# Kernel tuning notes

Hardware: AMD Instinct MI355X
Metric: run time of the kernel (lower is better)

Reference implementation:

```python
import jax, jax.numpy as jnp
import numpy as np

N_NODES = 50000
N_EDGES = 1600000


def setup_inputs() -> dict:
    key = jax.random.key(0)
    ks = jax.random.split(key, 12)
    x = jax.random.normal(ks[0], (N_NODES, 128), dtype=jnp.float32)
    edge_index = jax.random.randint(ks[1], (2, N_EDGES), 0, N_NODES, dtype=jnp.int32)
    edge_weight = jax.random.uniform(ks[2], (N_EDGES,), dtype=jnp.float32)
    K = 3
    def glorot(k, kk, cin, cout):
        s = (6.0 / (cin + cout)) ** 0.5
        return jax.random.uniform(k, (kk, cin, cout), dtype=jnp.float32, minval=-s, maxval=s)
    W0 = glorot(ks[3], K, 128, 128); b0 = jnp.zeros((128,), jnp.float32)
    W1 = glorot(ks[4], K, 128, 128); b1 = jnp.zeros((128,), jnp.float32)
    W2 = glorot(ks[5], K, 128, 64);  b2 = jnp.zeros((64,), jnp.float32)
    return {"x": x, "edge_index": edge_index, "edge_weight": edge_weight,
            "W0": W0, "b0": b0, "W1": W1, "b1": b1, "W2": W2, "b2": b2}


def _laplacian_norm(edge_index, edge_weight, n_nodes):
    # PyG ChebConv with lambda_max=2.0, sym normalization:
    # L_hat = 2*(I - D^-1/2 A D^-1/2)/lambda_max - I = -D^-1/2 A D^-1/2 (zero diag)
    src, dst = edge_index[0], edge_index[1]
    deg = jax.ops.segment_sum(edge_weight, src, num_segments=n_nodes)
    dinv = jnp.where(deg > 0, jax.lax.rsqrt(jnp.maximum(deg, 1e-30)), 0.0)
    return -dinv[src] * edge_weight * dinv[dst]


def _spmm(norm, src, dst, x, n_nodes):
    # out[i] = sum_{e: dst[e]=i} norm[e] * x[src[e]]
    return jax.ops.segment_sum(norm[:, None] * x[src], dst, num_segments=n_nodes)


def _cheb_conv(x, src, dst, norm, W, b, n_nodes):
    K = W.shape[0]
    out = jnp.einsum('nc,cd->nd', x, W[0])
    tx0 = x
    tx1 = _spmm(norm, src, dst, x, n_nodes)  # L_hat @ x
    out = out + jnp.einsum('nc,cd->nd', tx1, W[1])
    for k in range(2, K):
        tx2 = 2.0 * _spmm(norm, src, dst, tx1, n_nodes) - tx0
        out = out + jnp.einsum('nc,cd->nd', tx2, W[k])
        tx0, tx1 = tx1, tx2
    return out + b


def reference(x, edge_index, edge_weight, W0, b0, W1, b1, W2, b2):
    n_nodes = x.shape[0]
    src, dst = edge_index[0], edge_index[1]
    norm = _laplacian_norm(edge_index, edge_weight, n_nodes)
    h = jax.nn.sigmoid(_cheb_conv(x, src, dst, norm, W0, b0, n_nodes))
    h = jax.nn.sigmoid(_cheb_conv(h, src, dst, norm, W1, b1, n_nodes))
    return jax.nn.sigmoid(_cheb_conv(h, src, dst, norm, W2, b2, n_nodes))
```

## Files before the change

kernel.cpp:

```cpp
#include <hip/hip_runtime.h>
#include <hip/hip_fp16.h>
#include <math.h>

#define N_NODES 50000
#define N_EDGES 1600000
#define NBUCK 196
#define EBLK 400
#define CHUNK 4000

typedef _Float16 f16x8 __attribute__((ext_vector_type(8)));
typedef _Float16 f16x4 __attribute__((ext_vector_type(4)));
typedef _Float16 f16x2 __attribute__((ext_vector_type(2)));
typedef float f32x4 __attribute__((ext_vector_type(4)));

union HBits { __half h; unsigned short u; };

__global__ __launch_bounds__(256) void k_bcount(const int* __restrict__ src,
                                                const int* __restrict__ dst,
                                                int* __restrict__ bcnt_d,
                                                int* __restrict__ bcnt_s) {
    __shared__ int lcd[256];
    __shared__ int lcs[256];
    int tid = threadIdx.x;
    lcd[tid] = 0; lcs[tid] = 0;
    __syncthreads();
    int base = blockIdx.x * CHUNK;
    for (int i = tid; i < CHUNK; i += 256) {
        atomicAdd(&lcd[dst[base + i] >> 8], 1);
        atomicAdd(&lcs[src[base + i] >> 8], 1);
    }
    __syncthreads();
    bcnt_d[blockIdx.x * 256 + tid] = lcd[tid];
    bcnt_s[blockIdx.x * 256 + tid] = lcs[tid];
}

__global__ __launch_bounds__(256) void k_bscan1(int* __restrict__ bcnt_d,
                                                int* __restrict__ bcnt_s,
                                                int* __restrict__ btot) {
    int b = blockIdx.x & 255;
    int* bcnt = (blockIdx.x >> 8) ? bcnt_s : bcnt_d;
    int tid = threadIdx.x;
    int k0 = 2 * tid;
    int v0 = (k0 < EBLK) ? bcnt[k0 * 256 + b] : 0;
    int v1 = (k0 + 1 < EBLK) ? bcnt[(k0 + 1) * 256 + b] : 0;
    int pair = v0 + v1;
    __shared__ int s[256];
    s[tid] = pair;
    __syncthreads();
    for (int off = 1; off < 256; off <<= 1) {
        int t = (tid >= off) ? s[tid - off] : 0;
        __syncthreads();
        s[tid] += t;
        __syncthreads();
    }
    int excl = s[tid] - pair;
    if (k0 < EBLK)     bcnt[k0 * 256 + b] = excl;
    if (k0 + 1 < EBLK) bcnt[(k0 + 1) * 256 + b] = excl + v0;
    if (tid == 255) btot[(blockIdx.x >> 8) * 256 + b] = s[255];
}

__global__ __launch_bounds__(256) void k_bscan2(const int* __restrict__ btot,
                                                int* __restrict__ bstart_d,
                                                int* __restrict__ bstart_s,
                                                int* __restrict__ row_start) {
    __shared__ int s[256];
    int b = threadIdx.x;
    int v = btot[b];
    s[b] = v;
    __syncthreads();
    for (int off = 1; off < 256; off <<= 1) {
        int t = (b >= off) ? s[b - off] : 0;
        __syncthreads();
        s[b] += t;
        __syncthreads();
    }
    bstart_d[b] = s[b] - v;
    if (b == 0) {
        bstart_d[256] = N_EDGES;
        row_start[N_NODES] = N_EDGES;
    }
    __syncthreads();
    int v2 = btot[256 + b];
    s[b] = v2;
    __syncthreads();
    for (int off = 1; off < 256; off <<= 1) {
        int t = (b >= off) ? s[b - off] : 0;
        __syncthreads();
        s[b] += t;
        __syncthreads();
    }
    bstart_s[b] = s[b] - v2;
    if (b == 0) bstart_s[256] = N_EDGES;
}

__global__ __launch_bounds__(256) void k_bscatter(const int* __restrict__ src,
                                                  const int* __restrict__ dst,
                                                  const float* __restrict__ w,
                                                  const int* __restrict__ bcnt_d,
                                                  const int* __restrict__ bcnt_s,
                                                  const int* __restrict__ bstart_d,
                                                  const int* __restrict__ bstart_s,
                                                  uint2* __restrict__ dsw,
                                                  unsigned* __restrict__ ssw) {
    __shared__ int curd[256];
    __shared__ int curs[256];
    int tid = threadIdx.x;
    curd[tid] = bcnt_d[blockIdx.x * 256 + tid] + bstart_d[tid];
    curs[tid] = bcnt_s[blockIdx.x * 256 + tid] + bstart_s[tid];
    __syncthreads();
    int base = blockIdx.x * CHUNK;
    for (int i = tid; i < CHUNK; i += 256) {
        int d = dst[base + i];
        int ss = src[base + i];
        float wi = w[base + i];
        int p = atomicAdd(&curd[d >> 8], 1);
        uint2 r; r.x = (unsigned)ss | ((unsigned)(d & 255) << 16);
        r.y = __float_as_uint(wi);
        dsw[p] = r;
        int q = atomicAdd(&curs[ss >> 8], 1);
        HBits hw; hw.h = __float2half(wi);
        ssw[q] = (unsigned)(ss & 255) | ((unsigned)hw.u << 16);
    }
}

__global__ __launch_bounds__(256) void k_sdeg(const unsigned* __restrict__ ssw,
                                              const int* __restrict__ bstart_s,
                                              float* __restrict__ dinv) {
    __shared__ float h[256];
    int tid = threadIdx.x;
    int b = blockIdx.x;
    h[tid] = 0.f;
    __syncthreads();
    int e0 = bstart_s[b], e1 = bstart_s[b + 1];
    for (int i = e0 + tid; i < e1; i += 256) {
        unsigned r = ssw[i];
        HBits hb; hb.u = (unsigned short)(r >> 16);
        atomicAdd(&h[r & 255], __half2float(hb.h));
    }
    __syncthreads();
    int node = (b << 8) + tid;
    if (node < N_NODES) {
        float d = h[tid];
        dinv[node] = d > 0.f ? rsqrtf(fmaxf(d, 1e-30f)) : 0.f;
    }
}

__global__ __launch_bounds__(256) void k_bcsr(const uint2* __restrict__ dsw,
                                              const int* __restrict__ bstart_d,
                                              const float* __restrict__ dinv,
                                              int* __restrict__ row_start,
                                              unsigned* __restrict__ csr4) {
    __shared__ int ncnt[256];
    __shared__ int cur[256];
    __shared__ int sc[256];
    __shared__ float ldinv[256];
    int tid = threadIdx.x;
    int b = blockIdx.x;
    int node = (b << 8) + tid;
    ncnt[tid] = 0;
    ldinv[tid] = (node < N_NODES) ? dinv[node] : 0.f;
    __syncthreads();
    int e0 = bstart_d[b], e1 = bstart_d[b + 1];
    for (int i = e0 + tid; i < e1; i += 256)
        atomicAdd(&ncnt[(dsw[i].x >> 16) & 255], 1);
    __syncthreads();
    int v = ncnt[tid];
    sc[tid] = v;
    __syncthreads();
    for (int off = 1; off < 256; off <<= 1) {
        int t = (tid >= off) ? sc[tid - off] : 0;
        __syncthreads();
        sc[tid] += t;
        __syncthreads();
    }
    int excl = sc[tid] - v;
    cur[tid] = excl;
    if (node < N_NODES) row_start[node] = e0 + excl;
    __syncthreads();
    for (int i = e0 + tid; i < e1; i += 256) {
        uint2 sw = dsw[i];
        int srcn = sw.x & 0xFFFF;
        int ld = (sw.x >> 16) & 255;
        int p = e0 + atomicAdd(&cur[ld], 1);
        float nv = -dinv[srcn] * __uint_as_float(sw.y) * ldinv[ld];
        HBits hb; hb.h = __float2half(nv);
        csr4[p] = (unsigned)srcn | ((unsigned)hb.u << 16);
    }
}

__global__ void k_cvt_x(const float* __restrict__ x, __half* __restrict__ X, int n4) {
    int i = blockIdx.x * blockDim.x + threadIdx.x;
    if (i < n4) {
        float4 v = *(const float4*)&x[(size_t)i * 4];
        f16x4 o;
        o[0] = (_Float16)v.x; o[1] = (_Float16)v.y;
        o[2] = (_Float16)v.z; o[3] = (_Float16)v.w;
        *(f16x4*)&X[(size_t)i * 4] = o;
    }
}

__global__ void k_wt(const float* __restrict__ W, __half* __restrict__ Wt, int C) {
    int i = blockIdx.x * blockDim.x + threadIdx.x;
    if (i < 3 * C * 128) {
        int n = i >> 7, k = i & 127;
        int slice = n / C, c = n % C;
        float v;
        if (slice == 0)      v = 2.f * W[(size_t)(256 + k) * C + c];
        else if (slice == 1) v = W[(size_t)(128 + k) * C + c];
        else                 v = W[(size_t)k * C + c] - W[(size_t)(256 + k) * C + c];
        Wt[i] = __float2half(v);
    }
}

template <int ST_IN, int ST_ADD, int ST_OUT, int FW, int SIG, int F32>
__global__ __launch_bounds__(256) void k_spmm(const __half* __restrict__ Xin,
                                              const __half* __restrict__ Add,
                                              void* __restrict__ outp,
                                              const float* __restrict__ bias,
                                              const int* __restrict__ row_start,
                                              const unsigned* __restrict__ csr4) {
    constexpr int NL = FW / 8;
    constexpr int EG = 64 / NL;
    constexpr int KP2 = 16 / EG;
    int node = blockIdx.x * 4 + (threadIdx.x >> 6);
    int lane = threadIdx.x & 63;
    int eg = lane / NL;
    int fs = lane % NL;
    int s = row_start[node];
    int e = row_start[node + 1];
    const unsigned* cb = csr4 + eg;
    const __half* Tbase = Xin + fs * 8;
    float acc[8];
    #pragma unroll
    for (int f = 0; f < 8; f++) acc[f] = 0.f;

    int j = s;
    for (; j + 32 <= e; j += 32) {
        unsigned ea[KP2], eb[KP2];
        #pragma unroll
        for (int k = 0; k < KP2; k++) {
            ea[k] = cb[j + 2 * EG * k];
            eb[k] = cb[j + 2 * EG * k + EG];
        }
        f16x8 r0[KP2], r1[KP2]; f16x2 nv2[KP2];
        #pragma unroll
        for (int k = 0; k < KP2; k++) {
            int sp0 = (int)(ea[k] & 0xFFFFu);
            int sp1 = (int)(eb[k] & 0xFFFFu);
            r0[k] = *(const f16x8*)&Tbase[(size_t)sp0 * ST_IN];
            r1[k] = *(const f16x8*)&Tbase[(size_t)sp1 * ST_IN];
            unsigned np = (ea[k] >> 16) | (eb[k] & 0xFFFF0000u);
            __builtin_memcpy(&nv2[k], &np, 4);
        }
        #pragma unroll
        for (int k = 0; k < KP2; k++)
            #pragma unroll
            for (int f = 0; f < 8; f++) {
                f16x2 h; h[0] = r0[k][f]; h[1] = r1[k][f];
                acc[f] = __builtin_amdgcn_fdot2(h, nv2[k], acc[f], false);
            }
    }
    if (j + 16 <= e) {
        unsigned ea[KP2 / 2], eb[KP2 / 2];
        #pragma unroll
        for (int k = 0; k < KP2 / 2; k++) {
            ea[k] = cb[j + 2 * EG * k];
            eb[k] = cb[j + 2 * EG * k + EG];
        }
        #pragma unroll
        for (int k = 0; k < KP2 / 2; k++) {
            int sp0 = (int)(ea[k] & 0xFFFFu);
            int sp1 = (int)(eb[k] & 0xFFFFu);
            f16x8 r0 = *(const f16x8*)&Tbase[(size_t)sp0 * ST_IN];
            f16x8 r1 = *(const f16x8*)&Tbase[(size_t)sp1 * ST_IN];
            unsigned np = (ea[k] >> 16) | (eb[k] & 0xFFFF0000u);
            f16x2 nv; __builtin_memcpy(&nv, &np, 4);
            #pragma unroll
            for (int f = 0; f < 8; f++) {
                f16x2 h; h[0] = r0[f]; h[1] = r1[f];
                acc[f] = __builtin_amdgcn_fdot2(h, nv, acc[f], false);
            }
        }
        j += 16;
    }
    if (j < e) {
        #pragma unroll
        for (int k = 0; k < KP2 / 2; k++) {
            int i0 = j + 2 * EG * k + eg;
            int i1 = i0 + EG;
            unsigned va = csr4[min(i0, e - 1)];
            unsigned vb = csr4[min(i1, e - 1)];
            int sp0 = (int)(va & 0xFFFFu);
            int sp1 = (int)(vb & 0xFFFFu);
            unsigned np = (va >> 16) | (vb & 0xFFFF0000u);
            if (i0 >= e) np &= 0xFFFF0000u;
            if (i1 >= e) np &= 0x0000FFFFu;
            f16x2 nv; __builtin_memcpy(&nv, &np, 4);
            f16x8 r0 = *(const f16x8*)&Tbase[(size_t)sp0 * ST_IN];
            f16x8 r1 = *(const f16x8*)&Tbase[(size_t)sp1 * ST_IN];
            #pragma unroll
            for (int f = 0; f < 8; f++) {
                f16x2 h; h[0] = r0[f]; h[1] = r1[f];
                acc[f] = __builtin_amdgcn_fdot2(h, nv, acc[f], false);
            }
        }
    }
    #pragma unroll
    for (int f = 0; f < 8; f++)
        for (int m = NL; m < 64; m <<= 1)
            acc[f] += __shfl_xor(acc[f], m);
    if (eg == 0) {
        f16x8 av = *(const f16x8*)&Add[(size_t)node * ST_ADD + fs * 8];
        float v[8];
        #pragma unroll
        for (int f = 0; f < 8; f++) v[f] = acc[f] + (float)av[f];
        if (SIG) {
            #pragma unroll
            for (int f = 0; f < 8; f++) {
                v[f] += bias[fs * 8 + f];
                v[f] = 1.f / (1.f + expf(-v[f]));
            }
        }
        if (F32) {
            float* o = (float*)outp + (size_t)node * ST_OUT + fs * 8;
            float4 o0; o0.x = v[0]; o0.y = v[1]; o0.z = v[2]; o0.w = v[3];
            float4 o1; o1.x = v[4]; o1.y = v[5]; o1.z = v[6]; o1.w = v[7];
            *(float4*)&o[0] = o0;
            *(float4*)&o[4] = o1;
        } else {
            f16x8 o;
            #pragma unroll
            for (int f = 0; f < 8; f++) o[f] = (_Float16)v[f];
            *(f16x8*)((__half*)outp + (size_t)node * ST_OUT + fs * 8) = o;
        }
    }
}

template <int CC, int STG>
__global__ __launch_bounds__(256) void k_gemm(const __half* __restrict__ A,
                                              const __half* __restrict__ Wt,
                                              __half* __restrict__ G, int M) {
    constexpr int N3 = 3 * CC;
    constexpr int NF = N3 / 16;
    __shared__ _Float16 As[64][40];
    __shared__ _Float16 Bs[N3][40];
    int tid = threadIdx.x;
    int wave = tid >> 6, lane = tid & 63;
    int lm = lane & 15, lq = lane >> 4;
    int m0 = blockIdx.x * 64;
    f32x4 acc[NF];
    for (int nf = 0; nf < NF; nf++) acc[nf] = (f32x4)0.0f;

    for (int k0 = 0; k0 < 128; k0 += 32) {
        {
            int r = tid >> 2, q = tid & 3;
            int row = m0 + r;
            if (row >= M) row = M - 1;
            *(f16x8*)&As[r][q * 8] = *(const f16x8*)&A[(size_t)row * 128 + k0 + q * 8];
        }
        for (int i = 0; i < N3 / 64; i++) {
            int idx = tid + i * 256;
            int n = idx >> 2, q = idx & 3;
            *(f16x8*)&Bs[n][q * 8] = *(const f16x8*)&Wt[(size_t)n * 128 + k0 + q * 8];
        }
        __syncthreads();
        f16x8 a = *(const f16x8*)&As[wave * 16 + lm][lq * 8];
        for (int nf = 0; nf < NF; nf++) {
            f16x8 b = *(const f16x8*)&Bs[nf * 16 + lm][lq * 8];
            acc[nf] = __builtin_amdgcn_mfma_f32_16x16x32_f16(a, b, acc[nf], 0, 0, 0);
        }
        __syncthreads();
    }
    for (int nf = 0; nf < NF; nf++) {
        for (int r = 0; r < 4; r++) {
            int grow = m0 + wave * 16 + lq * 4 + r;
            int col = nf * 16 + lm;
            if (grow < M)
                G[(size_t)grow * STG + col] = __float2half(acc[nf][r]);
        }
    }
}

extern "C" void kernel_launch(void* const* d_in, const int* in_sizes, int n_in,
                              void* d_out, int out_size, void* d_ws, size_t ws_size,
                              hipStream_t stream) {
    const float* x  = (const float*)d_in[0];
    const int*   ei = (const int*)d_in[1];
    const float* ew = (const float*)d_in[2];
    const float* W0 = (const float*)d_in[3];
    const float* b0 = (const float*)d_in[4];
    const float* W1 = (const float*)d_in[5];
    const float* b1 = (const float*)d_in[6];
    const float* W2 = (const float*)d_in[7];
    const float* b2 = (const float*)d_in[8];
    const int* src = ei;
    const int* dst = ei + N_EDGES;

    char* ws = (char*)d_ws;
    size_t off = 0;
    auto alloc = [&](size_t bytes) -> char* {
        size_t p = (off + 255) & ~(size_t)255;
        off = p + bytes;
        return ws + p;
    };
    __half*   X      = (__half*)alloc((size_t)N_NODES * 128 * 2);
    __half*   G      = (__half*)alloc((size_t)N_NODES * 512 * 2);
    __half*   TMP    = (__half*)alloc((size_t)N_NODES * 128 * 2);
    unsigned* csr4   = (unsigned*)alloc((size_t)N_EDGES * 4);
    uint2*    dsw    = (uint2*)alloc((size_t)N_EDGES * 8);
    unsigned* ssw    = (unsigned*)alloc((size_t)N_EDGES * 4);
    int*      bcnt_d = (int*)alloc((size_t)EBLK * 256 * 4);
    int*      bcnt_s = (int*)alloc((size_t)EBLK * 256 * 4);
    int*      btot   = (int*)alloc(512 * 4);
    int*      bstart_d = (int*)alloc(257 * 4);
    int*      bstart_s = (int*)alloc(257 * 4);
    int*      row_start= (int*)alloc((size_t)(N_NODES + 1) * 4);
    float*    dinv   = (float*)alloc((size_t)N_NODES * 4);
    __half*   Wt0    = (__half*)alloc((size_t)384 * 128 * 2);
    __half*   Wt1    = (__half*)alloc((size_t)384 * 128 * 2);
    __half*   Wt2    = (__half*)alloc((size_t)192 * 128 * 2);

    k_bcount<<<EBLK, 256, 0, stream>>>(src, dst, bcnt_d, bcnt_s);
    k_bscan1<<<512, 256, 0, stream>>>(bcnt_d, bcnt_s, btot);
    k_bscan2<<<1, 256, 0, stream>>>(btot, bstart_d, bstart_s, row_start);
    k_bscatter<<<EBLK, 256, 0, stream>>>(src, dst, ew, bcnt_d, bcnt_s,
                                         bstart_d, bstart_s, dsw, ssw);
    k_sdeg<<<NBUCK, 256, 0, stream>>>(ssw, bstart_s, dinv);
    k_bcsr<<<NBUCK, 256, 0, stream>>>(dsw, bstart_d, dinv, row_start, csr4);

    k_cvt_x<<<(N_NODES * 32 + 255) / 256, 256, 0, stream>>>(x, X, N_NODES * 32);
    k_wt<<<(3 * 128 * 128 + 255) / 256, 256, 0, stream>>>(W0, Wt0, 128);
    k_wt<<<(3 * 128 * 128 + 255) / 256, 256, 0, stream>>>(W1, Wt1, 128);
    k_wt<<<(3 * 64 * 128 + 255) / 256, 256, 0, stream>>>(W2, Wt2, 64);

    int gb = (N_NODES + 63) / 64;
    int sb = N_NODES / 4;
    k_gemm<128, 512><<<gb, 256, 0, stream>>>(X, Wt0, G, N_NODES);
    k_spmm<512, 512, 128, 128, 0, 0><<<sb, 256, 0, stream>>>(G, G + 128, TMP,
                                                             nullptr, row_start, csr4);
    k_spmm<128, 512, 128, 128, 1, 0><<<sb, 256, 0, stream>>>(TMP, G + 256, X,
                                                             b0, row_start, csr4);
    k_gemm<128, 512><<<gb, 256, 0, stream>>>(X, Wt1, G, N_NODES);
    k_spmm<512, 512, 128, 128, 0, 0><<<sb, 256, 0, stream>>>(G, G + 128, TMP,
                                                             nullptr, row_start, csr4);
    k_spmm<128, 512, 128, 128, 1, 0><<<sb, 256, 0, stream>>>(TMP, G + 256, X,
                                                             b1, row_start, csr4);
    k_gemm<64, 256><<<gb, 256, 0, stream>>>(X, Wt2, G, N_NODES);
    k_spmm<256, 256, 64, 64, 0, 0><<<sb, 256, 0, stream>>>(G, G + 64, TMP,
                                                           nullptr, row_start, csr4);
    k_spmm<64, 256, 64, 64, 1, 1><<<sb, 256, 0, stream>>>(TMP, G + 128, d_out,
                                                          b2, row_start, csr4);
}
```

Before: 494.6 us.

## Pad CSR rows to multiples of eight and vectorize edge loads in SpMM

Each node's CSR row is padded to a multiple of 8 entries, with zero-weight filler entries and per-bucket slack. Row offsets and padded lengths are stored as a uint2 per node, which lets the SpMM read edges with aligned uint4/uint2 vector loads and drop the masked, clamped tail path. The three weight-transform kernels and the x conversion are also merged into one prep launch. The cost is a slightly larger CSR array and extra gathers of node 0 for the padding entries.

```diff
diff --git a/kernel.cpp b/kernel.cpp
--- a/kernel.cpp
+++ b/kernel.cpp
@@ -7,6 +7,7 @@
 #define NBUCK 196
 #define EBLK 400
 #define CHUNK 4000
+#define CSR_CAP (N_EDGES + 2048 * NBUCK + 4096)
 
 typedef _Float16 f16x8 __attribute__((ext_vector_type(8)));
 typedef _Float16 f16x4 __attribute__((ext_vector_type(4)));
@@ -61,8 +62,7 @@
 
 __global__ __launch_bounds__(256) void k_bscan2(const int* __restrict__ btot,
                                                 int* __restrict__ bstart_d,
-                                                int* __restrict__ bstart_s,
-                                                int* __restrict__ row_start) {
+                                                int* __restrict__ bstart_s) {
     __shared__ int s[256];
     int b = threadIdx.x;
     int v = btot[b];
@@ -75,10 +75,7 @@
         __syncthreads();
     }
     bstart_d[b] = s[b] - v;
-    if (b == 0) {
-        bstart_d[256] = N_EDGES;
-        row_start[N_NODES] = N_EDGES;
-    }
+    if (b == 0) bstart_d[256] = N_EDGES;
     __syncthreads();
     int v2 = btot[256 + b];
     s[b] = v2;
@@ -148,7 +145,7 @@
 __global__ __launch_bounds__(256) void k_bcsr(const uint2* __restrict__ dsw,
                                               const int* __restrict__ bstart_d,
                                               const float* __restrict__ dinv,
-                                              int* __restrict__ row_start,
+                                              uint2* __restrict__ ri,
                                               unsigned* __restrict__ csr4) {
     __shared__ int ncnt[256];
     __shared__ int cur[256];
@@ -165,7 +162,8 @@
         atomicAdd(&ncnt[(dsw[i].x >> 16) & 255], 1);
     __syncthreads();
     int v = ncnt[tid];
-    sc[tid] = v;
+    int pc = (v + 7) & ~7;
+    sc[tid] = pc;
     __syncthreads();
     for (int off = 1; off < 256; off <<= 1) {
         int t = (tid >= off) ? sc[tid - off] : 0;
@@ -173,42 +171,74 @@
         sc[tid] += t;
         __syncthreads();
     }
-    int excl = sc[tid] - v;
+    int excl = sc[tid] - pc;
     cur[tid] = excl;
-    if (node < N_NODES) row_start[node] = e0 + excl;
+    int pbase = ((e0 + 7) & ~7) + 2048 * b;
+    if (node < N_NODES) {
+        uint2 r; r.x = (unsigned)(pbase + excl); r.y = (unsigned)pc;
+        ri[node] = r;
+    }
     __syncthreads();
     for (int i = e0 + tid; i < e1; i += 256) {
         uint2 sw = dsw[i];
         int srcn = sw.x & 0xFFFF;
         int ld = (sw.x >> 16) & 255;
-        int p = e0 + atomicAdd(&cur[ld], 1);
+        int p = pbase + atomicAdd(&cur[ld], 1);
         float nv = -dinv[srcn] * __uint_as_float(sw.y) * ldinv[ld];
         HBits hb; hb.h = __float2half(nv);
         csr4[p] = (unsigned)srcn | ((unsigned)hb.u << 16);
     }
-}
-
-__global__ void k_cvt_x(const float* __restrict__ x, __half* __restrict__ X, int n4) {
-    int i = blockIdx.x * blockDim.x + threadIdx.x;
-    if (i < n4) {
+    __syncthreads();
+    int st = pbase + excl;
+    for (int i = v; i < pc; i++) csr4[st + i] = 0u;
+}
+
+__device__ inline void wt_one(const float* __restrict__ W, __half* __restrict__ Wt,
+                              int C, int i) {
+    int n = i >> 7, k = i & 127;
+    int slice = n / C, c = n % C;
+    float v;
+    if (slice == 0)      v = 2.f * W[(size_t)(256 + k) * C + c];
+    else if (slice == 1) v = W[(size_t)(128 + k) * C + c];
+    else                 v = W[(size_t)k * C + c] - W[(size_t)(256 + k) * C + c];
+    Wt[i] = __float2half(v);
+}
+
+__global__ __launch_bounds__(256) void k_prep(const float* __restrict__ x,
+                                              __half* __restrict__ X,
+                                              const float* __restrict__ W0,
+                                              const float* __restrict__ W1,
+                                              const float* __restrict__ W2,
+                                              __half* __restrict__ Wt0,
+                                              __half* __restrict__ Wt1,
+                                              __half* __restrict__ Wt2) {
+    int bid = blockIdx.x, tid = threadIdx.x;
+    if (bid < 6250) {
+        int i = bid * 256 + tid;
         float4 v = *(const float4*)&x[(size_t)i * 4];
         f16x4 o;
         o[0] = (_Float16)v.x; o[1] = (_Float16)v.y;
         o[2] = (_Float16)v.z; o[3] = (_Float16)v.w;
         *(f16x4*)&X[(size_t)i * 4] = o;
-    }
-}
-
-__global__ void k_wt(const float* __restrict__ W, __half* __restrict__ Wt, int C) {
-    int i = blockIdx.x * blockDim.x + threadIdx.x;
-    if (i < 3 * C * 128) {
-        int n = i >> 7, k = i & 127;
-        int slice = n / C, c = n % C;
-        float v;
-        if (slice == 0)      v = 2.f * W[(size_t)(256 + k) * C + c];
-        else if (slice == 1) v = W[(size_t)(128 + k) * C + c];
-        else                 v = W[(size_t)k * C + c] - W[(size_t)(256 + k) * C + c];
-        Wt[i] = __float2half(v);
+    } else if (bid < 6250 + 192) {
+        wt_one(W0, Wt0, 128, (bid - 6250) * 256 + tid);
+    } else if (bid < 6250 + 384) {
+        wt_one(W1, Wt1, 128, (bid - 6250 - 192) * 256 + tid);
+    } else {
+        wt_one(W2, Wt2, 64, (bid - 6250 - 384) * 256 + tid);
+    }
+}
+
+__device__ inline void mac_pair(const __half* __restrict__ Tbase, unsigned ea,
+                                unsigned eb, int stin, float acc[8]) {
+    f16x8 r0 = *(const f16x8*)&Tbase[(size_t)(ea & 0xFFFFu) * stin];
+    f16x8 r1 = *(const f16x8*)&Tbase[(size_t)(eb & 0xFFFFu) * stin];
+    unsigned np = (ea >> 16) | (eb & 0xFFFF0000u);
+    f16x2 nv; __builtin_memcpy(&nv, &np, 4);
+    #pragma unroll
+    for (int f = 0; f < 8; f++) {
+        f16x2 h; h[0] = r0[f]; h[1] = r1[f];
+        acc[f] = __builtin_amdgcn_fdot2(h, nv, acc[f], false);
     }
 }
 
@@ -217,92 +247,88 @@
                                               const __half* __restrict__ Add,
                                               void* __restrict__ outp,
                                               const float* __restrict__ bias,
-                                              const int* __restrict__ row_start,
+                                              const uint2* __restrict__ ri,
                                               const unsigned* __restrict__ csr4) {
     constexpr int NL = FW / 8;
     constexpr int EG = 64 / NL;
-    constexpr int KP2 = 16 / EG;
     int node = blockIdx.x * 4 + (threadIdx.x >> 6);
     int lane = threadIdx.x & 63;
     int eg = lane / NL;
     int fs = lane % NL;
-    int s = row_start[node];
-    int e = row_start[node + 1];
-    const unsigned* cb = csr4 + eg;
+    uint2 rv = ri[node];
+    int s = (int)rv.x;
+    int e = s + (int)rv.y;
     const __half* Tbase = Xin + fs * 8;
     float acc[8];
     #pragma unroll
     for (int f = 0; f < 8; f++) acc[f] = 0.f;
 
     int j = s;
-    for (; j + 32 <= e; j += 32) {
-        unsigned ea[KP2], eb[KP2];
-        #pragma unroll
-        for (int k = 0; k < KP2; k++) {
-            ea[k] = cb[j + 2 * EG * k];
-            eb[k] = cb[j + 2 * EG * k + EG];
-        }
-        f16x8 r0[KP2], r1[KP2]; f16x2 nv2[KP2];
-        #pragma unroll
-        for (int k = 0; k < KP2; k++) {
-            int sp0 = (int)(ea[k] & 0xFFFFu);
-            int sp1 = (int)(eb[k] & 0xFFFFu);
-            r0[k] = *(const f16x8*)&Tbase[(size_t)sp0 * ST_IN];
-            r1[k] = *(const f16x8*)&Tbase[(size_t)sp1 * ST_IN];
-            unsigned np = (ea[k] >> 16) | (eb[k] & 0xFFFF0000u);
-            __builtin_memcpy(&nv2[k], &np, 4);
-        }
-        #pragma unroll
-        for (int k = 0; k < KP2; k++)
-            #pragma unroll
-            for (int f = 0; f < 8; f++) {
-                f16x2 h; h[0] = r0[k][f]; h[1] = r1[k][f];
-                acc[f] = __builtin_amdgcn_fdot2(h, nv2[k], acc[f], false);
+    if (EG == 4) {
+        for (; j + 32 <= e; j += 32) {
+            uint4 c0 = *(const uint4*)&csr4[j + 4 * eg];
+            uint4 c1 = *(const uint4*)&csr4[j + 16 + 4 * eg];
+            unsigned ea[4] = {c0.x, c0.z, c1.x, c1.z};
+            unsigned eb[4] = {c0.y, c0.w, c1.y, c1.w};
+            f16x8 r0[4], r1[4];
+            #pragma unroll
+            for (int k = 0; k < 4; k++) {
+                r0[k] = *(const f16x8*)&Tbase[(size_t)(ea[k] & 0xFFFFu) * ST_IN];
+                r1[k] = *(const f16x8*)&Tbase[(size_t)(eb[k] & 0xFFFFu) * ST_IN];
             }
-    }
-    if (j + 16 <= e) {
-        unsigned ea[KP2 / 2], eb[KP2 / 2];
-        #pragma unroll
-        for (int k = 0; k < KP2 / 2; k++) {
-            ea[k] = cb[j + 2 * EG * k];
-            eb[k] = cb[j + 2 * EG * k + EG];
-        }
-        #pragma unroll
-        for (int k = 0; k < KP2 / 2; k++) {
-            int sp0 = (int)(ea[k] & 0xFFFFu);
-            int sp1 = (int)(eb[k] & 0xFFFFu);
-            f16x8 r0 = *(const f16x8*)&Tbase[(size_t)sp0 * ST_IN];
-            f16x8 r1 = *(const f16x8*)&Tbase[(size_t)sp1 * ST_IN];
-            unsigned np = (ea[k] >> 16) | (eb[k] & 0xFFFF0000u);
-            f16x2 nv; __builtin_memcpy(&nv, &np, 4);
-            #pragma unroll
-            for (int f = 0; f < 8; f++) {
-                f16x2 h; h[0] = r0[f]; h[1] = r1[f];
-                acc[f] = __builtin_amdgcn_fdot2(h, nv, acc[f], false);
+            #pragma unroll
+            for (int k = 0; k < 4; k++) {
+                unsigned np = (ea[k] >> 16) | (eb[k] & 0xFFFF0000u);
+                f16x2 nv; __builtin_memcpy(&nv, &np, 4);
+                #pragma unroll
+                for (int f = 0; f < 8; f++) {
+                    f16x2 h; h[0] = r0[k][f]; h[1] = r1[k][f];
+                    acc[f] = __builtin_amdgcn_fdot2(h, nv, acc[f], false);
+                }
             }
         }
-        j += 16;
-    }
-    if (j < e) {
-        #pragma unroll
-        for (int k = 0; k < KP2 / 2; k++) {
-            int i0 = j + 2 * EG * k + eg;
-            int i1 = i0 + EG;
-            unsigned va = csr4[min(i0, e - 1)];
-            unsigned vb = csr4[min(i1, e - 1)];
-            int sp0 = (int)(va & 0xFFFFu);
-            int sp1 = (int)(vb & 0xFFFFu);
-            unsigned np = (va >> 16) | (vb & 0xFFFF0000u);
-            if (i0 >= e) np &= 0xFFFF0000u;
-            if (i1 >= e) np &= 0x0000FFFFu;
-            f16x2 nv; __builtin_memcpy(&nv, &np, 4);
-            f16x8 r0 = *(const f16x8*)&Tbase[(size_t)sp0 * ST_IN];
-            f16x8 r1 = *(const f16x8*)&Tbase[(size_t)sp1 * ST_IN];
-            #pragma unroll
-            for (int f = 0; f < 8; f++) {
-                f16x2 h; h[0] = r0[f]; h[1] = r1[f];
-                acc[f] = __builtin_amdgcn_fdot2(h, nv, acc[f], false);
+        if (j + 16 <= e) {
+            uint4 c0 = *(const uint4*)&csr4[j + 4 * eg];
+            mac_pair(Tbase, c0.x, c0.y, ST_IN, acc);
+            mac_pair(Tbase, c0.z, c0.w, ST_IN, acc);
+            j += 16;
+        }
+        if (j + 8 <= e) {
+            uint2 c = *(const uint2*)&csr4[j + 2 * eg];
+            mac_pair(Tbase, c.x, c.y, ST_IN, acc);
+        }
+    } else {
+        for (; j + 32 <= e; j += 32) {
+            uint4 c0 = *(const uint4*)&csr4[j + 4 * eg];
+            unsigned ea[2] = {c0.x, c0.z};
+            unsigned eb[2] = {c0.y, c0.w};
+            f16x8 r0[2], r1[2];
+            #pragma unroll
+            for (int k = 0; k < 2; k++) {
+                r0[k] = *(const f16x8*)&Tbase[(size_t)(ea[k] & 0xFFFFu) * ST_IN];
+                r1[k] = *(const f16x8*)&Tbase[(size_t)(eb[k] & 0xFFFFu) * ST_IN];
             }
+            #pragma unroll
+            for (int k = 0; k < 2; k++) {
+                unsigned np = (ea[k] >> 16) | (eb[k] & 0xFFFF0000u);
+                f16x2 nv; __builtin_memcpy(&nv, &np, 4);
+                #pragma unroll
+                for (int f = 0; f < 8; f++) {
+                    f16x2 h; h[0] = r0[k][f]; h[1] = r1[k][f];
+                    acc[f] = __builtin_amdgcn_fdot2(h, nv, acc[f], false);
+                }
+            }
+        }
+        if (j + 16 <= e) {
+            uint2 c = *(const uint2*)&csr4[j + 2 * eg];
+            mac_pair(Tbase, c.x, c.y, ST_IN, acc);
+            j += 16;
+        }
+        if (j + 8 <= e) {
+            uint2 c = *(const uint2*)&csr4[j + 2 * (eg & 3)];
+            unsigned ea = c.x, eb = c.y;
+            if (eg >= 4) { ea &= 0xFFFFu; eb &= 0xFFFFu; }
+            mac_pair(Tbase, ea, eb, ST_IN, acc);
         }
     }
     #pragma unroll
@@ -406,7 +432,8 @@
     __half*   X      = (__half*)alloc((size_t)N_NODES * 128 * 2);
     __half*   G      = (__half*)alloc((size_t)N_NODES * 512 * 2);
     __half*   TMP    = (__half*)alloc((size_t)N_NODES * 128 * 2);
-    unsigned* csr4   = (unsigned*)alloc((size_t)N_EDGES * 4);
+    unsigned* csr4   = (unsigned*)alloc((size_t)CSR_CAP * 4);
+    uint2*    ri     = (uint2*)alloc((size_t)N_NODES * 8);
     uint2*    dsw    = (uint2*)alloc((size_t)N_EDGES * 8);
     unsigned* ssw    = (unsigned*)alloc((size_t)N_EDGES * 4);
     int*      bcnt_d = (int*)alloc((size_t)EBLK * 256 * 4);
@@ -414,7 +441,6 @@
     int*      btot   = (int*)alloc(512 * 4);
     int*      bstart_d = (int*)alloc(257 * 4);
     int*      bstart_s = (int*)alloc(257 * 4);
-    int*      row_start= (int*)alloc((size_t)(N_NODES + 1) * 4);
     float*    dinv   = (float*)alloc((size_t)N_NODES * 4);
     __half*   Wt0    = (__half*)alloc((size_t)384 * 128 * 2);
     __half*   Wt1    = (__half*)alloc((size_t)384 * 128 * 2);
@@ -422,32 +448,29 @@
 
     k_bcount<<<EBLK, 256, 0, stream>>>(src, dst, bcnt_d, bcnt_s);
     k_bscan1<<<512, 256, 0, stream>>>(bcnt_d, bcnt_s, btot);
-    k_bscan2<<<1, 256, 0, stream>>>(btot, bstart_d, bstart_s, row_start);
+    k_bscan2<<<1, 256, 0, stream>>>(btot, bstart_d, bstart_s);
     k_bscatter<<<EBLK, 256, 0, stream>>>(src, dst, ew, bcnt_d, bcnt_s,
                                          bstart_d, bstart_s, dsw, ssw);
     k_sdeg<<<NBUCK, 256, 0, stream>>>(ssw, bstart_s, dinv);
-    k_bcsr<<<NBUCK, 256, 0, stream>>>(dsw, bstart_d, dinv, row_start, csr4);
-
-    k_cvt_x<<<(N_NODES * 32 + 255) / 256, 256, 0, stream>>>(x, X, N_NODES * 32);
-    k_wt<<<(3 * 128 * 128 + 255) / 256, 256, 0, stream>>>(W0, Wt0, 128);
-    k_wt<<<(3 * 128 * 128 + 255) / 256, 256, 0, stream>>>(W1, Wt1, 128);
-    k_wt<<<(3 * 64 * 128 + 255) / 256, 256, 0, stream>>>(W2, Wt2, 64);
+    k_bcsr<<<NBUCK, 256, 0, stream>>>(dsw, bstart_d, dinv, ri, csr4);
+
+    k_prep<<<6250 + 192 + 192 + 96, 256, 0, stream>>>(x, X, W0, W1, W2, Wt0, Wt1, Wt2);
 
     int gb = (N_NODES + 63) / 64;
     int sb = N_NODES / 4;
     k_gemm<128, 512><<<gb, 256, 0, stream>>>(X, Wt0, G, N_NODES);
     k_spmm<512, 512, 128, 128, 0, 0><<<sb, 256, 0, stream>>>(G, G + 128, TMP,
-                                                             nullptr, row_start, csr4);
+                                                             nullptr, ri, csr4);
     k_spmm<128, 512, 128, 128, 1, 0><<<sb, 256, 0, stream>>>(TMP, G + 256, X,
-                                                             b0, row_start, csr4);
+                                                             b0, ri, csr4);
     k_gemm<128, 512><<<gb, 256, 0, stream>>>(X, Wt1, G, N_NODES);
     k_spmm<512, 512, 128, 128, 0, 0><<<sb, 256, 0, stream>>>(G, G + 128, TMP,
-                                                             nullptr, row_start, csr4);
+                                                             nullptr, ri, csr4);
     k_spmm<128, 512, 128, 128, 1, 0><<<sb, 256, 0, stream>>>(TMP, G + 256, X,
-                                                             b1, row_start, csr4);
+                                                             b1, ri, csr4);
     k_gemm<64, 256><<<gb, 256, 0, stream>>>(X, Wt2, G, N_NODES);
     k_spmm<256, 256, 64, 64, 0, 0><<<sb, 256, 0, stream>>>(G, G + 64, TMP,
-                                                           nullptr, row_start, csr4);
+                                                           nullptr, ri, csr4);
     k_spmm<64, 256, 64, 64, 1, 1><<<sb, 256, 0, stream>>>(TMP, G + 128, d_out,
-                                                          b2, row_start, csr4);
-}
+                                                          b2, ri, csr4);
+}
```

Result: no change. 487.2 us (-1.5%).
